# Performance work log

Measured on AMD Instinct MI355X. Metric: run time of the kernel, lower is better.

The kernel has to match this reference:

```python
import jax, jax.numpy as jnp
import numpy as np

B, S, D, H = 8, 2048, 64, 4
Dh = D // H  # head_dim = 16


def setup_inputs() -> dict:
    key = jax.random.key(0)
    k1, k2, k3, k4 = jax.random.split(key, 4)
    x = jax.random.normal(k1, (B, S, D), jnp.float32)
    # Linear weights stored torch-style as [out_features, in_features]
    W_qkv = jax.random.normal(k2, (3 * D, D), jnp.float32) * 0.125
    W_proj = jax.random.normal(k3, (D, D), jnp.float32) * 0.125
    b_proj = jnp.zeros((D,), jnp.float32)
    # Ragged structure: random valid length per sample, causal + padding mask
    lens = jax.random.randint(k4, (B,), S // 4, S + 1)
    pos = jnp.arange(S)
    key_valid = pos[None, :] < lens[:, None]          # [B, S]
    causal = pos[:, None] >= pos[None, :]             # [S, S]
    attn_mask = (causal[None, :, :] & key_valid[:, None, :])[:, None, :, :]  # [B,1,S,S], True=attend
    return {"x": x, "attn_mask": attn_mask, "W_qkv": W_qkv, "W_proj": W_proj, "b_proj": b_proj}


def reference(x, attn_mask, W_qkv, W_proj, b_proj):
    b, s, d = x.shape
    # fused QKV projection (qkv_bias=False)
    qkv = x @ W_qkv.T                                  # [B, S, 3D]
    qkv = qkv.reshape(b, s, 3, H, Dh).transpose(2, 0, 3, 1, 4)  # [3, B, H, S, Dh]
    q, k, v = qkv[0], qkv[1], qkv[2]
    scale = 1.0 / jnp.sqrt(jnp.asarray(Dh, x.dtype))
    scores = jnp.einsum('bhqd,bhkd->bhqk', q, k) * scale  # [B, H, S, S]
    neg = jnp.asarray(jnp.finfo(scores.dtype).min, scores.dtype)
    scores = jnp.where(attn_mask, scores, neg)
    attn = jax.nn.softmax(scores, axis=-1)
    ctx = jnp.einsum('bhqk,bhkd->bhqd', attn, v)       # [B, H, S, Dh]
    ctx = ctx.transpose(0, 2, 1, 3).reshape(b, s, d)   # [B, S, D]
    return ctx @ W_proj.T + b_proj
```

## Files before the change

### kernel.cpp

```cpp
#include <hip/hip_runtime.h>
#include <hip/hip_bf16.h>

typedef __attribute__((ext_vector_type(4))) float f32x4;
typedef __attribute__((ext_vector_type(16))) float f32x16;
typedef __attribute__((ext_vector_type(8))) short bf16x8;
typedef __attribute__((ext_vector_type(4))) short bf16x4;

#define SEQ 2048
#define NH 4
#define DH 16

#define WS_LEN 0
#define WS_WP  1024
#define WS_Q   65536
#define WS_K   (WS_Q + 2097152)
#define WS_V   (WS_K + 2097152)

#define MFMA16 __builtin_amdgcn_mfma_f32_16x16x32_bf16
#define MFMA32 __builtin_amdgcn_mfma_f32_32x32x16_bf16

__device__ __forceinline__ short f2bf(float f){
  __hip_bfloat16 h = __float2bfloat16(f);
  return __builtin_bit_cast(short, h);
}

__device__ __forceinline__ bf16x8 pack8(f32x4 a, f32x4 b){
  bf16x8 r;
  r[0]=f2bf(a[0]); r[1]=f2bf(a[1]); r[2]=f2bf(a[2]); r[3]=f2bf(a[3]);
  r[4]=f2bf(b[0]); r[5]=f2bf(b[1]); r[6]=f2bf(b[2]); r[7]=f2bf(b[3]);
  return r;
}

__global__ __launch_bounds__(256) void qkv_prep_kernel(const float* __restrict__ x,
                                                       const unsigned char* __restrict__ mask,
                                                       const float* __restrict__ wqkv,
                                                       const float* __restrict__ wproj,
                                                       unsigned char* __restrict__ ws){
  const int tid = threadIdx.x;
  if (blockIdx.x == 256){
    if (blockIdx.y == 1){
      short* wp = (short*)(ws + WS_WP);
      for (int i = tid; i < 64*64; i += 256) wp[i] = f2bf(wproj[i]);
      return;
    }
    const unsigned w0 = *(const unsigned*)mask;
    const int mode = (mask[2048] != 0) ? 0 : ((w0 == 1u) ? 1 : ((w0 == 0x3f800000u) ? 2 : 0));
    __shared__ int cnts[8];
    if (tid < 8) cnts[tid] = 0;
    __syncthreads();
    const int b = tid >> 5, j = tid & 31;
    const long long rowbase = (long long)b * SEQ * SEQ + (long long)(SEQ-1) * SEQ;
    int c = 0;
    if (mode == 0){
      const unsigned* mw = (const unsigned*)(mask + rowbase);
      for (int k = j; k < SEQ/4; k += 32){
        unsigned v = mw[k];
        c += (v & 0xffu ? 1:0) + (v & 0xff00u ? 1:0) + (v & 0xff0000u ? 1:0) + (v & 0xff000000u ? 1:0);
      }
    } else if (mode == 1){
      for (int k = j; k < SEQ; k += 32) c += ((const int*)mask)[rowbase + k] != 0;
    } else {
      for (int k = j; k < SEQ; k += 32) c += ((const float*)mask)[rowbase + k] != 0.0f;
    }
    atomicAdd(&cnts[b], c);
    __syncthreads();
    if (tid < 8) ((int*)ws)[tid] = cnts[tid];
    return;
  }

  const int lane = tid & 63;
  const int wv   = tid >> 6;
  const int c    = lane & 15;
  const int g    = lane >> 4;
  const int T0   = blockIdx.x * 64 + wv * 16;
  const f32x4 z = {0.f, 0.f, 0.f, 0.f};

  bf16x8 aw[2];
  {
    const float* xr = x + (long long)(T0 + c) * 64 + g * 8;
    #pragma unroll
    for (int w = 0; w < 2; ++w){
      f32x4 lo = *(const f32x4*)(xr + w*32);
      f32x4 hi = *(const f32x4*)(xr + w*32 + 4);
      aw[w] = pack8(lo, hi);
    }
  }

  const int tok  = T0 + c;
  const int b    = tok >> 11;
  const int s    = tok & (SEQ-1);
  short* Qd = (short*)(ws + WS_Q);
  short* Kd = (short*)(ws + WS_K);
  short* Vd = (short*)(ws + WS_V);

  #pragma unroll
  for (int oi = 0; oi < 6; ++oi){
    const int ot = blockIdx.y * 6 + oi;
    const float* wr = wqkv + (ot*16 + c) * 64 + g * 8;
    bf16x8 b0 = pack8(*(const f32x4*)(wr),      *(const f32x4*)(wr + 4));
    bf16x8 b1 = pack8(*(const f32x4*)(wr + 32), *(const f32x4*)(wr + 36));
    f32x4 acc = z;
    acc = MFMA16(b0, aw[0], acc, 0, 0, 0);
    acc = MFMA16(b1, aw[1], acc, 0, 0, 0);
    if (ot < 4){
      bf16x4 pk;
      #pragma unroll
      for (int r = 0; r < 4; ++r) pk[r] = f2bf(acc[r] * (0.25f * 1.44269504f));
      *(bf16x4*)(Qd + ((long long)(b*NH + ot) * SEQ + s) * DH + g*4) = pk;
    } else if (ot < 8){
      bf16x4 pk;
      #pragma unroll
      for (int r = 0; r < 4; ++r) pk[r] = f2bf(acc[r]);
      *(bf16x4*)(Kd + ((long long)(b*NH + (ot-4)) * SEQ + s) * DH + g*4) = pk;
    } else {
      #pragma unroll
      for (int r = 0; r < 4; ++r)
        Vd[((long long)(b*NH + (ot-8)) * DH + g*4 + r) * SEQ + s] = f2bf(acc[r]);
    }
  }
}

__global__ __launch_bounds__(512, 4) void attn_kernel(const unsigned char* __restrict__ ws,
                                                      const float* __restrict__ bproj,
                                                      float* __restrict__ out){
  const int tid  = threadIdx.x;
  const int lane = tid & 63;
  const int wv   = tid >> 6;
  const int h    = wv & 3;
  const int half = wv >> 2;
  const int c    = lane & 15;
  const int g    = lane >> 4;
  const int ql   = lane & 31;
  const int hi   = lane >> 5;
  const int L    = blockIdx.x;
  const int b    = (L + (L >> 8)) & 7;
  const int u    = L >> 3;
  const int t    = (u < 32) ? (2*u) : (63 - 2*(u - 32));
  const int q0   = t * 32;
  const int len  = ((const int*)ws)[b];
  const long long bh = (long long)(b*NH + h);
  const short* Q  = (const short*)(ws + WS_Q) + bh * SEQ * DH;
  const short* K  = (const short*)(ws + WS_K) + bh * SEQ * DH;
  const short* Vt = (const short*)(ws + WS_V) + bh * DH * SEQ;
  const short* Wp = (const short*)(ws + WS_WP);

  __shared__ __align__(16) unsigned char smem[78848];
  float* CMB = (float*)(smem + 65536);
  float* LSB = (float*)(smem + 74240);
  const unsigned pb   = (unsigned)wv * 8192;
  const unsigned CTXB = 74752;
  const f32x4 z  = {0.f,0.f,0.f,0.f};
  const f32x16 z16 = {0.f,0.f,0.f,0.f,0.f,0.f,0.f,0.f,0.f,0.f,0.f,0.f,0.f,0.f,0.f,0.f};
  const short one_bf = (short)0x3F80;
  const bf16x8 ones = {one_bf,one_bf,one_bf,one_bf,one_bf,one_bf,one_bf,one_bf};

  const bf16x8 qf = *(const bf16x8*)(Q + (q0 + ql)*DH + hi*8);

  f32x4 acc[2]  = {z, z};
  f32x4 accS[2] = {z, z};
  const int kcount = min(q0 + 32, len);
  const int nkt  = (kcount + 63) >> 6;
  const int icnt = min(q0 >> 6, len >> 6);
  const int nh0  = nkt >> 1;
  const int kb   = half ? nh0 : 0;
  const int ke   = half ? nkt : nh0;
  const int qg   = q0 + ql;
  const unsigned swq  = (unsigned)(ql & 7) << 4;
  const unsigned sw   = (unsigned)(c & 7) << 4;

  auto qkexp = [&](int tt, bf16x8 (&kk)[2]){
    const int k0 = tt * 64;
    const bool nomask = tt < icnt;
    const unsigned rowb = pb + ((unsigned)(tt & 1) << 12) + (unsigned)ql*128;
    #pragma unroll
    for (int kb32 = 0; kb32 < 2; ++kb32){
      f32x16 st = MFMA32(kk[kb32], qf, z16, 0, 0, 0);
      #pragma unroll
      for (int grp = 0; grp < 4; ++grp){
        const int keybase = kb32*32 + grp*8 + hi*4;
        float p0 = __builtin_amdgcn_exp2f(st[grp*4 + 0]);
        float p1 = __builtin_amdgcn_exp2f(st[grp*4 + 1]);
        float p2 = __builtin_amdgcn_exp2f(st[grp*4 + 2]);
        float p3 = __builtin_amdgcn_exp2f(st[grp*4 + 3]);
        if (!nomask){
          const int k = k0 + keybase;
          p0 = (k   <= qg && k   < len) ? p0 : 0.f;
          p1 = (k+1 <= qg && k+1 < len) ? p1 : 0.f;
          p2 = (k+2 <= qg && k+2 < len) ? p2 : 0.f;
          p3 = (k+3 <= qg && k+3 < len) ? p3 : 0.f;
        }
        uint2 pk;
        pk.x = __builtin_amdgcn_perm(__builtin_bit_cast(unsigned, p1),
                                     __builtin_bit_cast(unsigned, p0), 0x07060302u);
        pk.y = __builtin_amdgcn_perm(__builtin_bit_cast(unsigned, p3),
                                     __builtin_bit_cast(unsigned, p2), 0x07060302u);
        *(uint2*)&smem[rowb + ((unsigned)(keybase*2) ^ swq)] = pk;
      }
    }
  };

  bf16x8 knx[2], vcur[2], vnx[2], knn[2], vnn[2];
  if (kb < ke){
    const int k0 = kb * 64;
    bf16x8 k0f[2];
    k0f[0] = *(const bf16x8*)(K + (k0 + ql)*DH + hi*8);
    k0f[1] = *(const bf16x8*)(K + (k0 + 32 + ql)*DH + hi*8);
    vcur[0] = *(const bf16x8*)(Vt + c*SEQ + k0 + g*8);
    vcur[1] = *(const bf16x8*)(Vt + c*SEQ + k0 + 32 + g*8);
    qkexp(kb, k0f);
    if (kb + 1 < ke){
      const int k1 = k0 + 64;
      knx[0] = *(const bf16x8*)(K + (k1 + ql)*DH + hi*8);
      knx[1] = *(const bf16x8*)(K + (k1 + 32 + ql)*DH + hi*8);
      vnx[0] = *(const bf16x8*)(Vt + c*SEQ + k1 + g*8);
      vnx[1] = *(const bf16x8*)(Vt + c*SEQ + k1 + 32 + g*8);
    }
  }

  for (int kt = kb; kt < ke; ++kt){
    const unsigned bufr = pb + ((unsigned)(kt & 1) << 12);
    bf16x8 pa[2][2];
    #pragma unroll
    for (int qb = 0; qb < 2; ++qb)
      #pragma unroll
      for (int w = 0; w < 2; ++w)
        pa[qb][w] = *(const bf16x8*)&smem[bufr + (qb*16 + c)*128 + ((unsigned)(w*64 + g*16) ^ sw)];

    if (kt + 1 < ke){
      if (kt + 2 < ke){
        const int k2 = (kt + 2) * 64;
        knn[0] = *(const bf16x8*)(K + (k2 + ql)*DH + hi*8);
        knn[1] = *(const bf16x8*)(K + (k2 + 32 + ql)*DH + hi*8);
        vnn[0] = *(const bf16x8*)(Vt + c*SEQ + k2 + g*8);
        vnn[1] = *(const bf16x8*)(Vt + c*SEQ + k2 + 32 + g*8);
      }
      qkexp(kt + 1, knx);
    }

    #pragma unroll
    for (int qb = 0; qb < 2; ++qb)
      #pragma unroll
      for (int w = 0; w < 2; ++w){
        acc[qb]  = MFMA16(pa[qb][w], vcur[w], acc[qb], 0, 0, 0);
        accS[qb] = MFMA16(pa[qb][w], ones,    accS[qb], 0, 0, 0);
      }

    vcur[0] = vnx[0]; vcur[1] = vnx[1];
    knx[0] = knn[0]; knx[1] = knn[1];
    vnx[0] = vnn[0]; vnx[1] = vnn[1];
  }

  if (half == 0){
    #pragma unroll
    for (int qb = 0; qb < 2; ++qb){
      #pragma unroll
      for (int r = 0; r < 4; ++r)
        CMB[(h*32 + qb*16 + g*4 + r)*17 + c] = acc[qb][r];
      if (c == 0){
        #pragma unroll
        for (int r = 0; r < 4; ++r)
          LSB[h*32 + qb*16 + g*4 + r] = accS[qb][r];
      }
    }
  }
  __syncthreads();
  if (half == 1){
    #pragma unroll
    for (int qb = 0; qb < 2; ++qb){
      #pragma unroll
      for (int r = 0; r < 4; ++r){
        const int q = qb*16 + g*4 + r;
        const float tot = acc[qb][r] + CMB[(h*32 + q)*17 + c];
        const float lsT = LSB[h*32 + q] + accS[qb][r];
        const float cv  = tot / lsT;
        *(short*)&smem[CTXB + q*128 +
            (((unsigned)((h*16 + c)*2)) ^ ((unsigned)(q & 7) << 4))] = f2bf(cv);
      }
    }
  }
  __syncthreads();

  bf16x8 wpf[2];
  #pragma unroll
  for (int w = 0; w < 2; ++w)
    wpf[w] = *(const bf16x8*)(Wp + (h*16 + c)*64 + w*32 + g*8);
  const float bias = bproj[h*16 + c];
  f32x4 oa = z;
  const unsigned rbc = CTXB + (half*16 + c)*128;
  #pragma unroll
  for (int w = 0; w < 2; ++w){
    bf16x8 pa = *(const bf16x8*)&smem[rbc + ((unsigned)(w*64 + g*16) ^ sw)];
    oa = MFMA16(pa, wpf[w], oa, 0, 0, 0);
  }
  #pragma unroll
  for (int r = 0; r < 4; ++r)
    out[((long long)b * SEQ + q0 + half*16 + g*4 + r) * 64 + h*16 + c] = oa[r] + bias;
}

extern "C" void kernel_launch(void* const* d_in, const int* in_sizes, int n_in,
                              void* d_out, int out_size, void* d_ws, size_t ws_size,
                              hipStream_t stream) {
  const float* x     = (const float*)d_in[0];
  const unsigned char* mask = (const unsigned char*)d_in[1];
  const float* wqkv  = (const float*)d_in[2];
  const float* wproj = (const float*)d_in[3];
  const float* bproj = (const float*)d_in[4];
  float* out = (float*)d_out;
  unsigned char* ws = (unsigned char*)d_ws;

  qkv_prep_kernel<<<dim3(257, 2), 256, 0, stream>>>(x, mask, wqkv, wproj, ws);
  attn_kernel<<<512, 512, 0, stream>>>(ws, bproj, out);
}
```

Measured before the change: 32.08 us.

## Fuse QKV projection and attention into one kernel with per-batch grid barrier

Merges the QKV projection prep kernel and the attention kernel into a single launch. Each block projects 32 tokens, then signals a per-batch atomic counter and spins until all 64 blocks of its batch are done before starting attention. Each block computes the mask length itself, and W_proj is converted from fp32 on the fly instead of being pre-packed. This removes a kernel launch boundary and tail, but adds a memset, a spin-wait that relies on all blocks of a batch being co-resident, and redundant mask scanning per block.

```diff
diff --git a/kernel.cpp b/kernel.cpp
--- a/kernel.cpp
+++ b/kernel.cpp
@@ -10,11 +10,10 @@
 #define NH 4
 #define DH 16
 
-#define WS_LEN 0
-#define WS_WP  1024
-#define WS_Q   65536
-#define WS_K   (WS_Q + 2097152)
-#define WS_V   (WS_K + 2097152)
+#define WS_Q   0
+#define WS_K   2097152
+#define WS_V   4194304
+#define WS_CNT 6291456
 
 #define MFMA16 __builtin_amdgcn_mfma_f32_16x16x32_bf16
 #define MFMA32 __builtin_amdgcn_mfma_f32_32x32x16_bf16
@@ -31,126 +30,119 @@
   return r;
 }
 
-__global__ __launch_bounds__(256) void qkv_prep_kernel(const float* __restrict__ x,
-                                                       const unsigned char* __restrict__ mask,
-                                                       const float* __restrict__ wqkv,
-                                                       const float* __restrict__ wproj,
-                                                       unsigned char* __restrict__ ws){
-  const int tid = threadIdx.x;
-  if (blockIdx.x == 256){
-    if (blockIdx.y == 1){
-      short* wp = (short*)(ws + WS_WP);
-      for (int i = tid; i < 64*64; i += 256) wp[i] = f2bf(wproj[i]);
-      return;
-    }
-    const unsigned w0 = *(const unsigned*)mask;
-    const int mode = (mask[2048] != 0) ? 0 : ((w0 == 1u) ? 1 : ((w0 == 0x3f800000u) ? 2 : 0));
-    __shared__ int cnts[8];
-    if (tid < 8) cnts[tid] = 0;
-    __syncthreads();
-    const int b = tid >> 5, j = tid & 31;
-    const long long rowbase = (long long)b * SEQ * SEQ + (long long)(SEQ-1) * SEQ;
-    int c = 0;
-    if (mode == 0){
-      const unsigned* mw = (const unsigned*)(mask + rowbase);
-      for (int k = j; k < SEQ/4; k += 32){
-        unsigned v = mw[k];
-        c += (v & 0xffu ? 1:0) + (v & 0xff00u ? 1:0) + (v & 0xff0000u ? 1:0) + (v & 0xff000000u ? 1:0);
-      }
-    } else if (mode == 1){
-      for (int k = j; k < SEQ; k += 32) c += ((const int*)mask)[rowbase + k] != 0;
-    } else {
-      for (int k = j; k < SEQ; k += 32) c += ((const float*)mask)[rowbase + k] != 0.0f;
-    }
-    atomicAdd(&cnts[b], c);
-    __syncthreads();
-    if (tid < 8) ((int*)ws)[tid] = cnts[tid];
-    return;
-  }
-
+__global__ __launch_bounds__(512, 4) void fused_mha_kernel(
+    const float* __restrict__ x,
+    const unsigned char* __restrict__ mask,
+    const float* __restrict__ wqkv,
+    const float* __restrict__ wproj,
+    const float* __restrict__ bproj,
+    unsigned char* __restrict__ ws,
+    float* __restrict__ out)
+{
+  const int tid  = threadIdx.x;
   const int lane = tid & 63;
   const int wv   = tid >> 6;
   const int c    = lane & 15;
   const int g    = lane >> 4;
-  const int T0   = blockIdx.x * 64 + wv * 16;
-  const f32x4 z = {0.f, 0.f, 0.f, 0.f};
-
-  bf16x8 aw[2];
+  const int L    = blockIdx.x;
+  const int b    = (L + (L >> 8)) & 7;
+
+  __shared__ __align__(16) unsigned char smem[78864];
+  const f32x4 z  = {0.f,0.f,0.f,0.f};
+  const f32x16 z16 = {0.f,0.f,0.f,0.f,0.f,0.f,0.f,0.f,0.f,0.f,0.f,0.f,0.f,0.f,0.f,0.f};
+
   {
-    const float* xr = x + (long long)(T0 + c) * 64 + g * 8;
-    #pragma unroll
-    for (int w = 0; w < 2; ++w){
-      f32x4 lo = *(const f32x4*)(xr + w*32);
-      f32x4 hi = *(const f32x4*)(xr + w*32 + 4);
-      aw[w] = pack8(lo, hi);
-    }
-  }
-
-  const int tok  = T0 + c;
-  const int b    = tok >> 11;
-  const int s    = tok & (SEQ-1);
-  short* Qd = (short*)(ws + WS_Q);
-  short* Kd = (short*)(ws + WS_K);
-  short* Vd = (short*)(ws + WS_V);
-
-  #pragma unroll
-  for (int oi = 0; oi < 6; ++oi){
-    const int ot = blockIdx.y * 6 + oi;
-    const float* wr = wqkv + (ot*16 + c) * 64 + g * 8;
-    bf16x8 b0 = pack8(*(const f32x4*)(wr),      *(const f32x4*)(wr + 4));
-    bf16x8 b1 = pack8(*(const f32x4*)(wr + 32), *(const f32x4*)(wr + 36));
-    f32x4 acc = z;
-    acc = MFMA16(b0, aw[0], acc, 0, 0, 0);
-    acc = MFMA16(b1, aw[1], acc, 0, 0, 0);
-    if (ot < 4){
-      bf16x4 pk;
-      #pragma unroll
-      for (int r = 0; r < 4; ++r) pk[r] = f2bf(acc[r] * (0.25f * 1.44269504f));
-      *(bf16x4*)(Qd + ((long long)(b*NH + ot) * SEQ + s) * DH + g*4) = pk;
-    } else if (ot < 8){
-      bf16x4 pk;
-      #pragma unroll
-      for (int r = 0; r < 4; ++r) pk[r] = f2bf(acc[r]);
-      *(bf16x4*)(Kd + ((long long)(b*NH + (ot-4)) * SEQ + s) * DH + g*4) = pk;
-    } else {
-      #pragma unroll
-      for (int r = 0; r < 4; ++r)
-        Vd[((long long)(b*NH + (ot-8)) * DH + g*4 + r) * SEQ + s] = f2bf(acc[r]);
-    }
-  }
-}
-
-__global__ __launch_bounds__(512, 4) void attn_kernel(const unsigned char* __restrict__ ws,
-                                                      const float* __restrict__ bproj,
-                                                      float* __restrict__ out){
-  const int tid  = threadIdx.x;
-  const int lane = tid & 63;
-  const int wv   = tid >> 6;
+    const int tok16 = L * 32 + (wv & 1) * 16;
+    bf16x8 aw[2];
+    {
+      const float* xr = x + (long long)(tok16 + c) * 64 + g * 8;
+      #pragma unroll
+      for (int w = 0; w < 2; ++w){
+        f32x4 lo = *(const f32x4*)(xr + w*32);
+        f32x4 hi = *(const f32x4*)(xr + w*32 + 4);
+        aw[w] = pack8(lo, hi);
+      }
+    }
+    const int tok = tok16 + c;
+    const int bA  = tok >> 11;
+    const int s   = tok & (SEQ-1);
+    short* Qd = (short*)(ws + WS_Q);
+    short* Kd = (short*)(ws + WS_K);
+    short* Vd = (short*)(ws + WS_V);
+
+    #pragma unroll
+    for (int oi = 0; oi < 3; ++oi){
+      const int ot = (wv >> 1) * 3 + oi;
+      const float* wr = wqkv + (ot*16 + c) * 64 + g * 8;
+      bf16x8 b0 = pack8(*(const f32x4*)(wr),      *(const f32x4*)(wr + 4));
+      bf16x8 b1 = pack8(*(const f32x4*)(wr + 32), *(const f32x4*)(wr + 36));
+      f32x4 acc = z;
+      acc = MFMA16(b0, aw[0], acc, 0, 0, 0);
+      acc = MFMA16(b1, aw[1], acc, 0, 0, 0);
+      if (ot < 4){
+        bf16x4 pk;
+        #pragma unroll
+        for (int r = 0; r < 4; ++r) pk[r] = f2bf(acc[r] * (0.25f * 1.44269504f));
+        *(bf16x4*)(Qd + ((long long)(bA*NH + ot) * SEQ + s) * DH + g*4) = pk;
+      } else if (ot < 8){
+        bf16x4 pk;
+        #pragma unroll
+        for (int r = 0; r < 4; ++r) pk[r] = f2bf(acc[r]);
+        *(bf16x4*)(Kd + ((long long)(bA*NH + (ot-4)) * SEQ + s) * DH + g*4) = pk;
+      } else {
+        #pragma unroll
+        for (int r = 0; r < 4; ++r)
+          Vd[((long long)(bA*NH + (ot-8)) * DH + g*4 + r) * SEQ + s] = f2bf(acc[r]);
+      }
+    }
+
+    if (wv == 0){
+      const unsigned w0 = *(const unsigned*)mask;
+      const int mode = (mask[2048] != 0) ? 0 : ((w0 == 1u) ? 1 : ((w0 == 0x3f800000u) ? 2 : 0));
+      const long long rowbase = (long long)b * SEQ * SEQ + (long long)(SEQ-1) * SEQ;
+      int cnt = 0;
+      if (mode == 0){
+        const unsigned* mw = (const unsigned*)(mask + rowbase);
+        for (int k = lane; k < SEQ/4; k += 64){
+          unsigned v = mw[k];
+          cnt += (v & 0xffu ? 1:0) + (v & 0xff00u ? 1:0) + (v & 0xff0000u ? 1:0) + (v & 0xff000000u ? 1:0);
+        }
+      } else if (mode == 1){
+        for (int k = lane; k < SEQ; k += 64) cnt += ((const int*)mask)[rowbase + k] != 0;
+      } else {
+        for (int k = lane; k < SEQ; k += 64) cnt += ((const float*)mask)[rowbase + k] != 0.0f;
+      }
+      #pragma unroll
+      for (int off = 32; off >= 1; off >>= 1) cnt += __shfl_xor(cnt, off);
+      if (lane == 0) *(int*)(smem + 78848) = cnt;
+    }
+  }
+
+  __syncthreads();
+  if (tid == 0){
+    int* cnts = (int*)(ws + WS_CNT);
+    __hip_atomic_fetch_add(&cnts[L >> 6], 1, __ATOMIC_RELEASE, __HIP_MEMORY_SCOPE_AGENT);
+    while (__hip_atomic_load(&cnts[b], __ATOMIC_RELAXED, __HIP_MEMORY_SCOPE_AGENT) < 64)
+      __builtin_amdgcn_s_sleep(4);
+  }
+  __syncthreads();
+
+  const int len  = *(const int*)(smem + 78848);
   const int h    = wv & 3;
   const int half = wv >> 2;
-  const int c    = lane & 15;
-  const int g    = lane >> 4;
   const int ql   = lane & 31;
   const int hi   = lane >> 5;
-  const int L    = blockIdx.x;
-  const int b    = (L + (L >> 8)) & 7;
   const int u    = L >> 3;
   const int t    = (u < 32) ? (2*u) : (63 - 2*(u - 32));
   const int q0   = t * 32;
-  const int len  = ((const int*)ws)[b];
   const long long bh = (long long)(b*NH + h);
   const short* Q  = (const short*)(ws + WS_Q) + bh * SEQ * DH;
   const short* K  = (const short*)(ws + WS_K) + bh * SEQ * DH;
   const short* Vt = (const short*)(ws + WS_V) + bh * DH * SEQ;
-  const short* Wp = (const short*)(ws + WS_WP);
-
-  __shared__ __align__(16) unsigned char smem[78848];
   float* CMB = (float*)(smem + 65536);
   float* LSB = (float*)(smem + 74240);
   const unsigned pb   = (unsigned)wv * 8192;
   const unsigned CTXB = 74752;
-  const f32x4 z  = {0.f,0.f,0.f,0.f};
-  const f32x16 z16 = {0.f,0.f,0.f,0.f,0.f,0.f,0.f,0.f,0.f,0.f,0.f,0.f,0.f,0.f,0.f,0.f};
   const short one_bf = (short)0x3F80;
   const bf16x8 ones = {one_bf,one_bf,one_bf,one_bf,one_bf,one_bf,one_bf,one_bf};
 
@@ -281,9 +273,12 @@
   __syncthreads();
 
   bf16x8 wpf[2];
-  #pragma unroll
-  for (int w = 0; w < 2; ++w)
-    wpf[w] = *(const bf16x8*)(Wp + (h*16 + c)*64 + w*32 + g*8);
+  {
+    const float* wr = wproj + (h*16 + c)*64 + g*8;
+    #pragma unroll
+    for (int w = 0; w < 2; ++w)
+      wpf[w] = pack8(*(const f32x4*)(wr + w*32), *(const f32x4*)(wr + w*32 + 4));
+  }
   const float bias = bproj[h*16 + c];
   f32x4 oa = z;
   const unsigned rbc = CTXB + (half*16 + c)*128;
@@ -308,6 +303,6 @@
   float* out = (float*)d_out;
   unsigned char* ws = (unsigned char*)d_ws;
 
-  qkv_prep_kernel<<<dim3(257, 2), 256, 0, stream>>>(x, mask, wqkv, wproj, ws);
-  attn_kernel<<<512, 512, 0, stream>>>(ws, bproj, out);
+  hipMemsetAsync(ws + WS_CNT, 0, 32, stream);
+  fused_mha_kernel<<<512, 512, 0, stream>>>(x, mask, wqkv, wproj, bproj, ws, out);
 }
```

After: 62.95 us. 1.96x slower.
